# Kernel optimization log

Measured on AMD Instinct MI355X. Metric: run time of the kernel, lower is better.

## Reference

```python
import jax, jax.numpy as jnp
import numpy as np

B, T, D = 32, 2048, 80
K1 = K2 = 3
S1 = S2 = 2
CB_DIM, CB_SIZE = 512, 1024
MASK_P = 0.1
NOISE_STD = 0.1
INPUT_DIM = D * K1 * K2  # 720


def _win_idx(T_in, k, s):
    Tp = (T_in - k) // s + 1
    return jnp.arange(Tp)[:, None] * s + jnp.arange(k)[None, :]  # (Tp, k)


def _unfold(x, k, s):
    # matches torch x.unfold(1, k, s).view(B, Tp, -1): out[b, t, f*k + j] = x[b, t*s + j, f]
    idx = _win_idx(x.shape[1], k, s)
    w = x[:, idx, :]                 # (B, Tp, k, F)
    w = jnp.swapaxes(w, 2, 3)        # (B, Tp, F, k)
    return w.reshape(w.shape[0], w.shape[1], -1)


def setup_inputs() -> dict:
    key = jax.random.key(0)
    k1, k2, k3, k4, k5 = jax.random.split(key, 5)
    raw_feats = jax.random.normal(k1, (B, T, D), jnp.float32)
    auged_feats = jax.random.normal(k2, (B, T, D), jnp.float32)
    length = jax.random.randint(k3, (B,), T // 2, T + 1)
    xav = (2.0 / (INPUT_DIM + CB_DIM)) ** 0.5  # xavier_normal std
    projector = jax.random.normal(k4, (INPUT_DIM, CB_DIM), jnp.float32) * xav
    codebook = jax.random.normal(k5, (CB_SIZE, CB_DIM), jnp.float32)
    return {"raw_feats": raw_feats, "auged_feats": auged_feats, "length": length,
            "projector": projector, "codebook": codebook}


def reference(raw_feats, auged_feats, length, projector, codebook):
    T1 = (T - K1) // S1 + 1
    T2 = (T1 - K2) // S2 + 1
    idx1 = _win_idx(T, K1, S1)                         # (T1, K1)
    idx2 = _win_idx(T1, K2, S2)                        # (T2, K2)
    frame_windows = idx1[idx2].reshape(T2, K1 * K2)    # (T2, 9) original frame idx per subsampled step
    label_lengths = ((length - K1) // S1 + 1 - K2) // S2 + 1  # (B,)

    # --- label path: two torch-style unfolds -> project -> nearest codebook entry ---
    stacked = _unfold(_unfold(raw_feats, K1, S1), K2, S2)     # (B, T2, 720)
    targets = jnp.matmul(stacked, projector)                  # (B, T2, 512)
    # squared-euclidean expansion; same argmin as ||t - c||
    dist = (jnp.sum(targets * targets, axis=-1, keepdims=True)
            - 2.0 * jnp.einsum('btd,cd->btc', targets, codebook)
            + jnp.sum(codebook * codebook, axis=-1))          # (B, T2, 1024)
    labels = jnp.argmin(dist, axis=-1) + 1                    # labels start from 1; 0 = ignore idx
    valid = jnp.arange(T2)[None, :] < label_lengths[:, None]  # (B, T2)
    labels = jnp.where(valid, labels, 0)[None]                # (num_codebooks=1, B, T2)

    # --- static (span length 1) random masking on valid subsampled steps ---
    mkey = jax.random.key(42)
    km, kn = jax.random.split(mkey)
    masked = (jax.random.uniform(km, (B, T2)) < MASK_P) & valid
    masked_dim = masked.astype(jnp.float32)                   # (B, T2)
    # scatter masked subsampled steps back onto original frame indices (union of windows)
    hits = jnp.zeros((B, T), jnp.float32).at[:, frame_windows].add(masked_dim[:, :, None])
    frame_mask = hits > 0                                     # (B, T)
    noise = NOISE_STD * jax.random.normal(kn, (B, T, D), auged_feats.dtype)
    masked_feats = jnp.where(frame_mask[:, :, None], noise, auged_feats)
    return masked_feats, labels, masked_dim
```

## Files before the change

kernel.cpp:

```cpp
#include <hip/hip_runtime.h>
#include <cstdint>

#define B_    32
#define T_    2048
#define D_    80
#define T2_   511
#define NROW  16352
#define GK    720
#define CBD   512
#define CBS   1024
#define HMASK 8176
#define HN    2621440
#define NP    16384
#define KB    23

using bfrag = __attribute__((ext_vector_type(8))) short;
using f32x4 = __attribute__((ext_vector_type(4))) float;
using s8    = __attribute__((ext_vector_type(8))) short;

__device__ inline ushort f2bf(float f){
  uint32_t u = __float_as_uint(f);
  uint32_t r = (u + 0x7FFFu + ((u >> 16) & 1u)) >> 16;
  return (ushort)r;
}
__device__ inline float bf2f(ushort h){ return __uint_as_float(((uint32_t)h) << 16); }

#define GLL16(gsrc, ldst) __builtin_amdgcn_global_load_lds( \
    (__attribute__((address_space(1))) void*)(gsrc), \
    (__attribute__((address_space(3))) void*)(ldst), 16, 0, 0)

__host__ __device__ inline uint32_t rotl_(uint32_t v, int d){ return (v<<d)|(v>>(32-d)); }

__host__ __device__ inline void tf2x32(uint32_t k0, uint32_t k1, uint32_t& x0, uint32_t& x1){
  uint32_t ks2 = k0 ^ k1 ^ 0x1BD11BDAu;
  x0 += k0; x1 += k1;
  const int r0[4] = {13,15,26,6}, r1[4] = {17,29,16,24};
#pragma unroll
  for (int i=0;i<4;i++){ x0 += x1; x1 = rotl_(x1, r0[i]); x1 ^= x0; }
  x0 += k1; x1 += ks2 + 1u;
#pragma unroll
  for (int i=0;i<4;i++){ x0 += x1; x1 = rotl_(x1, r1[i]); x1 ^= x0; }
  x0 += ks2; x1 += k0 + 2u;
#pragma unroll
  for (int i=0;i<4;i++){ x0 += x1; x1 = rotl_(x1, r0[i]); x1 ^= x0; }
  x0 += k0; x1 += k1 + 3u;
#pragma unroll
  for (int i=0;i<4;i++){ x0 += x1; x1 = rotl_(x1, r1[i]); x1 ^= x0; }
  x0 += k1; x1 += ks2 + 4u;
#pragma unroll
  for (int i=0;i<4;i++){ x0 += x1; x1 = rotl_(x1, r0[i]); x1 ^= x0; }
  x0 += ks2; x1 += k0 + 5u;
}

__device__ inline float erfinv_f(float x){
  float w = -log1pf(-x*x);
  float p;
  if (w < 5.0f){
    w -= 2.5f;
    p = 2.81022636e-08f;
    p = fmaf(p, w, 3.43273939e-07f);
    p = fmaf(p, w, -3.5233877e-06f);
    p = fmaf(p, w, -4.39150654e-06f);
    p = fmaf(p, w, 0.00021858087f);
    p = fmaf(p, w, -0.00125372503f);
    p = fmaf(p, w, -0.00417768164f);
    p = fmaf(p, w, 0.246640727f);
    p = fmaf(p, w, 1.50140941f);
  } else {
    w = sqrtf(w) - 3.0f;
    p = -0.000200214257f;
    p = fmaf(p, w, 0.000100950558f);
    p = fmaf(p, w, 0.00134934322f);
    p = fmaf(p, w, -0.00367342844f);
    p = fmaf(p, w, 0.00573950773f);
    p = fmaf(p, w, -0.0076224613f);
    p = fmaf(p, w, 0.00943887047f);
    p = fmaf(p, w, 1.00167406f);
    p = fmaf(p, w, 2.83297682f);
  }
  return p * x;
}

__device__ inline int label_len(int L){ return (((L - 3) / 2) - 2) / 2 + 1; }

__global__ void cbnorm_k(const float* __restrict__ cb, ushort* __restrict__ W0, ushort* __restrict__ W1){
  int c = blockIdx.x, lane = threadIdx.x;
  double s = 0.0;
  for (int k = lane; k < CBD; k += 64){ float v = cb[c*CBD + k]; s += (double)v * (double)v; }
#pragma unroll
  for (int off = 32; off; off >>= 1) s += __shfl_down(s, off);
  float nf = (float)s;
  nf = __shfl(nf, 0);
  size_t base = ((size_t)(KB-1)*CBS + c)*32;
  int sw = ((c >> 1) & 3) << 3;
  if (lane == 16){
    float h = -0.5f * nf;
    ushort h0 = f2bf(h); ushort h1 = f2bf(h - bf2f(h0));
    W0[base + (16 ^ sw)] = h0; W1[base + (16 ^ sw)] = h1;
  } else if (lane > 16 && lane < 32){
    W0[base + (lane ^ sw)] = 0; W1[base + (lane ^ sw)] = 0;
  }
}

__global__ void gather_k(const float* __restrict__ raw, ushort* __restrict__ S0, ushort* __restrict__ S1){
  int idx = blockIdx.x * 256 + threadIdx.x;
  int g  = idx & 3;
  int n  = (idx >> 2) & (NP - 1);
  int kb = idx >> 16;
  int b = n / T2_, t2 = n - b * T2_;
  s8 o0, o1;
#pragma unroll
  for (int j = 0; j < 8; ++j){
    int k = kb*32 + g*8 + j;
    float v = 0.f;
    if (n < NROW){
      if (k < GK){
        int d = k / 9, rem = k - 9*d;
        int k1 = rem / 3, k2 = rem - 3*k1;
        int tm = 4*t2 + 2*k2 + k1;
        v = raw[(b * T_ + tm) * D_ + d];
      } else if (k == GK) v = 1.f;
    }
    ushort h0 = f2bf(v); ushort h1 = f2bf(v - bf2f(h0));
    o0[j] = (short)h0; o1[j] = (short)h1;
  }
  int gs = g ^ ((n >> 1) & 3);
  size_t off = ((size_t)kb*NP + n)*32 + gs*8;
  *(s8*)&S0[off] = o0;
  *(s8*)&S1[off] = o1;
}

__global__ __launch_bounds__(256) void wgemm_k(const float* __restrict__ P, const float* __restrict__ cb,
                                               float* __restrict__ Wp){
  __shared__ float sP[16][68];
  __shared__ float sC[16][68];
  int r0 = blockIdx.y * 64, c0 = blockIdx.x * 64;
  int kz = blockIdx.z;
  int tid = threadIdx.x, tx = tid & 15, ty = tid >> 4;
  float acc[4][4] = {};
  for (int k0 = kz * 128; k0 < kz * 128 + 128; k0 += 16){
    __syncthreads();
    {
      int r = tid >> 2, kq = tid & 3;
      int rr = r0 + r;
      float4 v = {0.f,0.f,0.f,0.f};
      if (rr < GK) v = *(const float4*)&P[rr * CBD + k0 + kq * 4];
      sP[kq*4+0][r] = v.x; sP[kq*4+1][r] = v.y; sP[kq*4+2][r] = v.z; sP[kq*4+3][r] = v.w;
      float4 w = *(const float4*)&cb[(c0 + r) * CBD + k0 + kq * 4];
      sC[kq*4+0][r] = w.x; sC[kq*4+1][r] = w.y; sC[kq*4+2][r] = w.z; sC[kq*4+3][r] = w.w;
    }
    __syncthreads();
#pragma unroll
    for (int kk = 0; kk < 16; ++kk){
      float4 a = *(const float4*)&sP[kk][ty * 4];
      float4 b = *(const float4*)&sC[kk][tx * 4];
      float av[4] = {a.x,a.y,a.z,a.w}, bv[4] = {b.x,b.y,b.z,b.w};
#pragma unroll
      for (int i = 0; i < 4; ++i)
#pragma unroll
        for (int j = 0; j < 4; ++j) acc[i][j] = fmaf(av[i], bv[j], acc[i][j]);
    }
  }
#pragma unroll
  for (int i = 0; i < 4; ++i){
    int r = r0 + ty * 4 + i;
    if (r < GK){
      float4 o; o.x = acc[i][0]; o.y = acc[i][1]; o.z = acc[i][2]; o.w = acc[i][3];
      *(float4*)&Wp[((size_t)kz * GK + r) * CBS + c0 + tx * 4] = o;
    }
  }
}

__global__ void wreduce_k(const float* __restrict__ Wp, ushort* __restrict__ W0, ushort* __restrict__ W1){
  int idx = blockIdx.x * 256 + threadIdx.x;
  int r = idx >> 10, c = idx & (CBS - 1);
  float v = Wp[(size_t)r * CBS + c]
          + Wp[((size_t)GK + r) * CBS + c]
          + Wp[((size_t)2*GK + r) * CBS + c]
          + Wp[((size_t)3*GK + r) * CBS + c];
  ushort h0 = f2bf(v); ushort h1 = f2bf(v - bf2f(h0));
  size_t o = ((size_t)(r >> 5) * CBS + c) * 32 + ((r & 31) ^ (((c >> 1) & 3) << 3));
  W0[o] = h0; W1[o] = h1;
}

__global__ __launch_bounds__(512, 2) void score_k(const ushort* __restrict__ S0, const ushort* __restrict__ S1,
                                                  const ushort* __restrict__ W0g, const ushort* __restrict__ W1g,
                                                  float* __restrict__ pval, int* __restrict__ pidx){
  __shared__ __align__(16) ushort lds[2 * 16384];
  int tid = threadIdx.x;
  int lane = tid & 63, wid = tid >> 6;
  int wm = wid >> 2, wn = wid & 3;
  int g = lane >> 4, lr = lane & 15;
  int gsw = g ^ ((lr >> 1) & 3);

  int id = blockIdx.x;
  int xcd = id & 7, slot = id >> 3;
  int cidx = slot & 3, ridx = (xcd << 3) | (slot >> 2);
  int n0 = ridx * 256, c0 = cidx * 256;

  const ushort* sbase = (wid < 4) ? (S0 + (size_t)n0*32) : (S1 + (size_t)n0*32);
  int ckbase  = (wid & 3) * 4;
  int dstbase = ((wid < 4) ? 0 : 8192) + ckbase * 512;

  size_t wofs0 = ((size_t)c0 + wn*64 + lr) * 32 + gsw * 8;

  f32x4 acc[8][4] = {};

#pragma unroll
  for (int q = 0; q < 4; ++q)
    GLL16(sbase + (size_t)(ckbase + q)*512 + lane*8, lds + dstbase + q*512);
  asm volatile("s_waitcnt vmcnt(0)" ::: "memory");
  __builtin_amdgcn_s_barrier();

  for (int kb = 0; kb < KB; ++kb){
    const ushort* cur = lds + ((kb & 1) ? 16384 : 0);
    ushort*       nxt = lds + ((kb & 1) ? 0 : 16384);

    bfrag b0c[4], b1c[4];
    {
      size_t wo = (size_t)kb * CBS * 32 + wofs0;
#pragma unroll
      for (int nt = 0; nt < 4; ++nt){
        b0c[nt] = *(const bfrag*)&W0g[wo + (size_t)nt*512];
        b1c[nt] = *(const bfrag*)&W1g[wo + (size_t)nt*512];
      }
    }
    if (kb + 1 < KB){
      const ushort* s = sbase + (size_t)(kb+1)*NP*32;
#pragma unroll
      for (int q = 0; q < 4; ++q)
        GLL16(s + (size_t)(ckbase + q)*512 + lane*8, nxt + dstbase + q*512);
    }
    bfrag a0[8], a1[8];
    {
      int abase = (wm*128 + lr)*32 + gsw*8;
#pragma unroll
      for (int mt = 0; mt < 8; ++mt){
        a0[mt] = *(const bfrag*)&cur[abase + mt*512];
        a1[mt] = *(const bfrag*)&cur[8192 + abase + mt*512];
      }
    }
#pragma unroll
    for (int hf = 0; hf < 2; ++hf){
      __builtin_amdgcn_s_setprio(1);
#pragma unroll
      for (int mtl = 0; mtl < 4; ++mtl)
#pragma unroll
        for (int nt = 0; nt < 4; ++nt)
          acc[hf*4+mtl][nt] = __builtin_amdgcn_mfma_f32_16x16x32_bf16(a0[hf*4+mtl], b0c[nt], acc[hf*4+mtl][nt], 0,0,0);
#pragma unroll
      for (int mtl = 0; mtl < 4; ++mtl)
#pragma unroll
        for (int nt = 0; nt < 4; ++nt)
          acc[hf*4+mtl][nt] = __builtin_amdgcn_mfma_f32_16x16x32_bf16(a0[hf*4+mtl], b1c[nt], acc[hf*4+mtl][nt], 0,0,0);
#pragma unroll
      for (int mtl = 0; mtl < 4; ++mtl)
#pragma unroll
        for (int nt = 0; nt < 4; ++nt)
          acc[hf*4+mtl][nt] = __builtin_amdgcn_mfma_f32_16x16x32_bf16(a1[hf*4+mtl], b0c[nt], acc[hf*4+mtl][nt], 0,0,0);
      __builtin_amdgcn_s_setprio(0);
    }
    asm volatile("s_waitcnt vmcnt(0)" ::: "memory");
    __builtin_amdgcn_s_barrier();
  }

#pragma unroll
  for (int mt = 0; mt < 8; ++mt){
    float bv[4]; int bi[4];
#pragma unroll
    for (int r = 0; r < 4; ++r){
      float best = 3.4e38f; int besti = 0;
#pragma unroll
      for (int nt = 0; nt < 4; ++nt){
        float d = -2.f * acc[mt][nt][r];
        int c = c0 + wn*64 + nt*16 + lr;
        if (d < best){ best = d; besti = c; }
      }
      bv[r] = best; bi[r] = besti;
    }
#pragma unroll
    for (int off = 1; off < 16; off <<= 1){
#pragma unroll
      for (int r = 0; r < 4; ++r){
        float ov = __shfl_xor(bv[r], off);
        int   oi = __shfl_xor(bi[r], off);
        if (ov < bv[r] || (ov == bv[r] && oi < bi[r])){ bv[r] = ov; bi[r] = oi; }
      }
    }
    if (lr == 0){
      int pp = cidx*4 + wn;
#pragma unroll
      for (int r = 0; r < 4; ++r){
        int n = n0 + wm*128 + mt*16 + g*4 + r;
        pval[(size_t)pp*NP + n] = bv[r];
        pidx[(size_t)pp*NP + n] = bi[r];
      }
    }
  }
}

__device__ inline void emit_mask(const int* len, float* md, int i, uint32_t bits){
  float u = __uint_as_float((bits >> 9) | 0x3F800000u) - 1.0f;
  int b = i / T2_, t2 = i - b * T2_;
  bool m = (u < 0.1f) && (t2 < label_len(len[b]));
  md[i] = m ? 1.0f : 0.0f;
}

__device__ inline void comb_one(const float* __restrict__ pval, const int* __restrict__ pidx,
                                const int* __restrict__ len, float* __restrict__ lb, int n){
  float bv = pval[n]; int bi = pidx[n];
#pragma unroll
  for (int p = 1; p < 16; ++p){
    float v = pval[(size_t)p*NP + n]; int ii = pidx[(size_t)p*NP + n];
    if (v < bv || (v == bv && ii < bi)){ bv = v; bi = ii; }
  }
  int b = n / T2_, t2 = n - b * T2_;
  lb[n] = (t2 < label_len(len[b])) ? (float)(bi + 1) : 0.f;
}

__global__ void maskcomb_k(const float* __restrict__ pval, const int* __restrict__ pidx,
                           const int* __restrict__ len, float* __restrict__ lb,
                           float* __restrict__ md, uint32_t km0, uint32_t km1){
  int j = blockIdx.x * 256 + threadIdx.x;
  if (j >= HMASK) return;
  uint32_t x0 = (uint32_t)j, x1 = (uint32_t)(j + HMASK);
  tf2x32(km0, km1, x0, x1);
  emit_mask(len, md, j, x0);
  emit_mask(len, md, j + HMASK, x1);
  comb_one(pval, pidx, len, lb, j);
  comb_one(pval, pidx, len, lb, j + HMASK);
}

__device__ inline bool frame_masked(const float* md, int i){
  int tabs = i / D_;
  int t = tabs & (T_ - 1);
  int b = i / (D_ * T_);
  int lo = (t < 3) ? 0 : ((t - 3) >> 2);
  int hi = t >> 2; if (hi > T2_ - 1) hi = T2_ - 1;
  bool m = false;
  for (int t2 = lo; t2 <= hi; ++t2) m = m || (md[b * T2_ + t2] != 0.f);
  return m;
}

__device__ inline float noise_from_bits(uint32_t bits){
  float f = __uint_as_float((bits >> 9) | 0x3F800000u) - 1.0f;
  const float LOV = -0.99999994f;
  float u = fmaf(f, 2.0f, LOV);
  u = fmaxf(LOV, u);
  return 0.1f * (1.41421356f * erfinv_f(u));
}

__global__ void feats_k(const float* __restrict__ aug, const float* __restrict__ md,
                        float* __restrict__ mf, uint32_t kn0, uint32_t kn1){
  int j = blockIdx.x * 256 + threadIdx.x;
  bool m1 = frame_masked(md, j);
  bool m2 = frame_masked(md, j + HN);
  if (m1 || m2){
    uint32_t x0 = (uint32_t)j, x1 = (uint32_t)(j + HN);
    tf2x32(kn0, kn1, x0, x1);
    mf[j]      = m1 ? noise_from_bits(x0) : aug[j];
    mf[j + HN] = m2 ? noise_from_bits(x1) : aug[j + HN];
  } else {
    mf[j]      = aug[j];
    mf[j + HN] = aug[j + HN];
  }
}

extern "C" void kernel_launch(void* const* d_in, const int* in_sizes, int n_in,
                              void* d_out, int out_size, void* d_ws, size_t ws_size,
                              hipStream_t stream){
  const float* raw  = (const float*)d_in[0];
  const float* aug  = (const float*)d_in[1];
  const int*   len  = (const int*)  d_in[2];
  const float* proj = (const float*)d_in[3];
  const float* cb   = (const float*)d_in[4];

  float* out = (float*)d_out;
  float* mf  = out;
  float* lb  = out + 5242880;
  float* md  = out + 5259232;

  ushort* w  = (ushort*)d_ws;
  ushort* W0 = w;
  ushort* W1 = W0 + (size_t)KB*CBS*32;
  ushort* S0 = W1 + (size_t)KB*CBS*32;
  ushort* S1 = S0 + (size_t)KB*NP*32;
  float* pval = (float*)(S1 + (size_t)KB*NP*32);
  int*   pidx = (int*)(pval + (size_t)16*NP);
  float* Wp   = (float*)(pidx + (size_t)16*NP);

  uint32_t a0 = 0u, a1 = 2u, b0 = 1u, b1 = 3u;
  tf2x32(0u, 42u, a0, a1);
  tf2x32(0u, 42u, b0, b1);
  uint32_t km0 = a0, km1 = b0, kn0 = a1, kn1 = b1;

  cbnorm_k<<<CBS, 64, 0, stream>>>(cb, W0, W1);
  wgemm_k<<<dim3(CBS / 64, 12, 4), 256, 0, stream>>>(proj, cb, Wp);
  wreduce_k<<<(GK * CBS) / 256, 256, 0, stream>>>(Wp, W0, W1);
  gather_k<<<(KB * NP * 4) / 256, 256, 0, stream>>>(raw, S0, S1);
  score_k<<<256, 512, 0, stream>>>(S0, S1, W0, W1, pval, pidx);
  maskcomb_k<<<(HMASK + 255) / 256, 256, 0, stream>>>(pval, pidx, len, lb, md, km0, km1);
  feats_k<<<HN / 256, 256, 0, stream>>>(aug, md, mf, kn0, kn1);
}
```

Before: 161.5 us.

## Stage codebook tiles in LDS for score GEMM and tile gather through shared memory

The score kernel now loads both the split-bf16 activation tiles and the split-bf16 weight tiles into a double-buffered 128KB dynamic LDS region. Previously each wave read the weight fragments straight from global memory. The MFMA loop is split into phases separated by sched and workgroup barriers, which lowers register pressure and reuses the A fragments. The gather kernel now stages a block of raw frames in LDS and has each thread write all k-blocks for its row, replacing the per-element strided global reads. This adds more barriers and LDS footprint, and occupancy may drop with 128KB of shared memory per block.

```diff
diff --git a/kernel.cpp b/kernel.cpp
--- a/kernel.cpp
+++ b/kernel.cpp
@@ -13,6 +13,7 @@
 #define HN    2621440
 #define NP    16384
 #define KB    23
+#define GLDS  (259*81*4)
 
 using bfrag = __attribute__((ext_vector_type(8))) short;
 using f32x4 = __attribute__((ext_vector_type(4))) float;
@@ -102,32 +103,46 @@
   }
 }
 
-__global__ void gather_k(const float* __restrict__ raw, ushort* __restrict__ S0, ushort* __restrict__ S1){
-  int idx = blockIdx.x * 256 + threadIdx.x;
-  int g  = idx & 3;
-  int n  = (idx >> 2) & (NP - 1);
-  int kb = idx >> 16;
-  int b = n / T2_, t2 = n - b * T2_;
-  s8 o0, o1;
-#pragma unroll
-  for (int j = 0; j < 8; ++j){
-    int k = kb*32 + g*8 + j;
-    float v = 0.f;
-    if (n < NROW){
+__global__ __launch_bounds__(256) void gather_k(const float* __restrict__ raw,
+                                                ushort* __restrict__ S0, ushort* __restrict__ S1){
+  extern __shared__ float lraw[];
+  int b = blockIdx.x >> 3, ch = blockIdx.x & 7;
+  int t20 = ch * 64;
+  int nt2 = (T2_ - t20 < 64) ? (T2_ - t20) : 64;
+  int r0 = 4 * t20;
+  int rows = (T_ - r0 < 259) ? (T_ - r0) : 259;
+  int tid = threadIdx.x;
+  const float4* gsrc = (const float4*)(raw + ((size_t)b*T_ + r0)*D_);
+  int nf4 = rows * 20;
+  for (int q = tid; q < nf4; q += 256){
+    float4 v = gsrc[q];
+    int row = q / 20, c4 = (q - row*20) * 4;
+    float* dst = &lraw[row*81 + c4];
+    dst[0]=v.x; dst[1]=v.y; dst[2]=v.z; dst[3]=v.w;
+  }
+  __syncthreads();
+  int nl = tid >> 2, g = tid & 3;
+  if (nl >= nt2) return;
+  int n = b*T2_ + t20 + nl;
+  int gs = g ^ ((n >> 1) & 3);
+  for (int kb = 0; kb < KB; ++kb){
+    s8 o0, o1;
+#pragma unroll
+    for (int j = 0; j < 8; ++j){
+      int k = kb*32 + g*8 + j;
+      float v = 0.f;
       if (k < GK){
         int d = k / 9, rem = k - 9*d;
         int k1 = rem / 3, k2 = rem - 3*k1;
-        int tm = 4*t2 + 2*k2 + k1;
-        v = raw[(b * T_ + tm) * D_ + d];
+        v = lraw[(4*nl + 2*k2 + k1)*81 + d];
       } else if (k == GK) v = 1.f;
-    }
-    ushort h0 = f2bf(v); ushort h1 = f2bf(v - bf2f(h0));
-    o0[j] = (short)h0; o1[j] = (short)h1;
-  }
-  int gs = g ^ ((n >> 1) & 3);
-  size_t off = ((size_t)kb*NP + n)*32 + gs*8;
-  *(s8*)&S0[off] = o0;
-  *(s8*)&S1[off] = o1;
+      ushort h0 = f2bf(v); ushort h1 = f2bf(v - bf2f(h0));
+      o0[j] = (short)h0; o1[j] = (short)h1;
+    }
+    size_t off = ((size_t)kb*NP + n)*32 + gs*8;
+    *(s8*)&S0[off] = o0;
+    *(s8*)&S1[off] = o1;
+  }
 }
 
 __global__ __launch_bounds__(256) void wgemm_k(const float* __restrict__ P, const float* __restrict__ cb,
@@ -184,9 +199,9 @@
 }
 
 __global__ __launch_bounds__(512, 2) void score_k(const ushort* __restrict__ S0, const ushort* __restrict__ S1,
-                                                  const ushort* __restrict__ W0g, const ushort* __restrict__ W1g,
+                                                  const ushort* __restrict__ W0, const ushort* __restrict__ W1,
                                                   float* __restrict__ pval, int* __restrict__ pidx){
-  __shared__ __align__(16) ushort lds[2 * 16384];
+  extern __shared__ ushort lds[];
   int tid = threadIdx.x;
   int lane = tid & 63, wid = tid >> 6;
   int wm = wid >> 2, wn = wid & 3;
@@ -198,70 +213,100 @@
   int cidx = slot & 3, ridx = (xcd << 3) | (slot >> 2);
   int n0 = ridx * 256, c0 = cidx * 256;
 
-  const ushort* sbase = (wid < 4) ? (S0 + (size_t)n0*32) : (S1 + (size_t)n0*32);
-  int ckbase  = (wid & 3) * 4;
-  int dstbase = ((wid < 4) ? 0 : 8192) + ckbase * 512;
-
-  size_t wofs0 = ((size_t)c0 + wn*64 + lr) * 32 + gsw * 8;
+  int p = wid >> 1, h = wid & 1;
+  const ushort* src0;
+  size_t kstride;
+  if      (p == 0){ src0 = S0 + (size_t)n0*32; kstride = (size_t)NP*32; }
+  else if (p == 1){ src0 = S1 + (size_t)n0*32; kstride = (size_t)NP*32; }
+  else if (p == 2){ src0 = W0 + (size_t)c0*32; kstride = (size_t)CBS*32; }
+  else            { src0 = W1 + (size_t)c0*32; kstride = (size_t)CBS*32; }
+  src0 += h * 4096;
+  int doff = p * 8192 + h * 4096;
 
   f32x4 acc[8][4] = {};
 
 #pragma unroll
-  for (int q = 0; q < 4; ++q)
-    GLL16(sbase + (size_t)(ckbase + q)*512 + lane*8, lds + dstbase + q*512);
-  asm volatile("s_waitcnt vmcnt(0)" ::: "memory");
-  __builtin_amdgcn_s_barrier();
+  for (int q = 0; q < 8; ++q) GLL16(src0 + q*512 + lane*8, lds + doff + q*512);
+
+  int abase = (wm*128 + lr)*32 + gsw*8;
+  int bbase = (wn*64  + lr)*32 + gsw*8;
 
   for (int kb = 0; kb < KB; ++kb){
-    const ushort* cur = lds + ((kb & 1) ? 16384 : 0);
-    ushort*       nxt = lds + ((kb & 1) ? 0 : 16384);
-
-    bfrag b0c[4], b1c[4];
-    {
-      size_t wo = (size_t)kb * CBS * 32 + wofs0;
-#pragma unroll
-      for (int nt = 0; nt < 4; ++nt){
-        b0c[nt] = *(const bfrag*)&W0g[wo + (size_t)nt*512];
-        b1c[nt] = *(const bfrag*)&W1g[wo + (size_t)nt*512];
-      }
-    }
-    if (kb + 1 < KB){
-      const ushort* s = sbase + (size_t)(kb+1)*NP*32;
-#pragma unroll
-      for (int q = 0; q < 4; ++q)
-        GLL16(s + (size_t)(ckbase + q)*512 + lane*8, nxt + dstbase + q*512);
-    }
-    bfrag a0[8], a1[8];
-    {
-      int abase = (wm*128 + lr)*32 + gsw*8;
-#pragma unroll
-      for (int mt = 0; mt < 8; ++mt){
-        a0[mt] = *(const bfrag*)&cur[abase + mt*512];
-        a1[mt] = *(const bfrag*)&cur[8192 + abase + mt*512];
-      }
-    }
-#pragma unroll
-    for (int hf = 0; hf < 2; ++hf){
-      __builtin_amdgcn_s_setprio(1);
-#pragma unroll
-      for (int mtl = 0; mtl < 4; ++mtl)
-#pragma unroll
-        for (int nt = 0; nt < 4; ++nt)
-          acc[hf*4+mtl][nt] = __builtin_amdgcn_mfma_f32_16x16x32_bf16(a0[hf*4+mtl], b0c[nt], acc[hf*4+mtl][nt], 0,0,0);
-#pragma unroll
-      for (int mtl = 0; mtl < 4; ++mtl)
-#pragma unroll
-        for (int nt = 0; nt < 4; ++nt)
-          acc[hf*4+mtl][nt] = __builtin_amdgcn_mfma_f32_16x16x32_bf16(a0[hf*4+mtl], b1c[nt], acc[hf*4+mtl][nt], 0,0,0);
-#pragma unroll
-      for (int mtl = 0; mtl < 4; ++mtl)
-#pragma unroll
-        for (int nt = 0; nt < 4; ++nt)
-          acc[hf*4+mtl][nt] = __builtin_amdgcn_mfma_f32_16x16x32_bf16(a1[hf*4+mtl], b0c[nt], acc[hf*4+mtl][nt], 0,0,0);
-      __builtin_amdgcn_s_setprio(0);
-    }
+    const ushort* cur = lds + (kb & 1) * 32768;
+    ushort*       nxt = lds + ((kb & 1) ^ 1) * 32768;
     asm volatile("s_waitcnt vmcnt(0)" ::: "memory");
     __builtin_amdgcn_s_barrier();
+
+    const ushort* A0 = cur;
+    const ushort* A1 = cur + 8192;
+    const ushort* B0 = cur + 16384;
+    const ushort* B1 = cur + 24576;
+
+    bfrag a[4], b0f[4], b1f[4];
+#pragma unroll
+    for (int mt = 0; mt < 4; ++mt) a[mt] = *(const bfrag*)&A0[abase + mt*512];
+#pragma unroll
+    for (int nt = 0; nt < 4; ++nt) b0f[nt] = *(const bfrag*)&B0[bbase + nt*512];
+    if (kb + 1 < KB){
+      const ushort* s = src0 + (size_t)(kb+1)*kstride;
+#pragma unroll
+      for (int q = 0; q < 8; ++q) GLL16(s + q*512 + lane*8, nxt + doff + q*512);
+    }
+    asm volatile("s_waitcnt lgkmcnt(0)" ::: "memory");
+    __builtin_amdgcn_sched_barrier(0);
+    __builtin_amdgcn_s_setprio(1);
+#pragma unroll
+    for (int mt = 0; mt < 4; ++mt)
+#pragma unroll
+      for (int nt = 0; nt < 4; ++nt)
+        acc[mt][nt] = __builtin_amdgcn_mfma_f32_16x16x32_bf16(a[mt], b0f[nt], acc[mt][nt], 0,0,0);
+    __builtin_amdgcn_s_setprio(0);
+    __builtin_amdgcn_sched_barrier(0);
+    __builtin_amdgcn_s_barrier();
+#pragma unroll
+    for (int nt = 0; nt < 4; ++nt) b1f[nt] = *(const bfrag*)&B1[bbase + nt*512];
+    asm volatile("s_waitcnt lgkmcnt(0)" ::: "memory");
+    __builtin_amdgcn_sched_barrier(0);
+    __builtin_amdgcn_s_setprio(1);
+#pragma unroll
+    for (int mt = 0; mt < 4; ++mt)
+#pragma unroll
+      for (int nt = 0; nt < 4; ++nt)
+        acc[mt][nt] = __builtin_amdgcn_mfma_f32_16x16x32_bf16(a[mt], b1f[nt], acc[mt][nt], 0,0,0);
+    __builtin_amdgcn_s_setprio(0);
+    __builtin_amdgcn_sched_barrier(0);
+    __builtin_amdgcn_s_barrier();
+#pragma unroll
+    for (int mt = 0; mt < 4; ++mt) a[mt] = *(const bfrag*)&A0[abase + (mt+4)*512];
+    asm volatile("s_waitcnt lgkmcnt(0)" ::: "memory");
+    __builtin_amdgcn_sched_barrier(0);
+    __builtin_amdgcn_s_setprio(1);
+#pragma unroll
+    for (int mt = 0; mt < 4; ++mt)
+#pragma unroll
+      for (int nt = 0; nt < 4; ++nt)
+        acc[4+mt][nt] = __builtin_amdgcn_mfma_f32_16x16x32_bf16(a[mt], b0f[nt], acc[4+mt][nt], 0,0,0);
+#pragma unroll
+    for (int mt = 0; mt < 4; ++mt)
+#pragma unroll
+      for (int nt = 0; nt < 4; ++nt)
+        acc[4+mt][nt] = __builtin_amdgcn_mfma_f32_16x16x32_bf16(a[mt], b1f[nt], acc[4+mt][nt], 0,0,0);
+    __builtin_amdgcn_s_setprio(0);
+    __builtin_amdgcn_sched_barrier(0);
+    __builtin_amdgcn_s_barrier();
+    bfrag a1f[8];
+#pragma unroll
+    for (int mt = 0; mt < 8; ++mt) a1f[mt] = *(const bfrag*)&A1[abase + mt*512];
+    asm volatile("s_waitcnt lgkmcnt(0)" ::: "memory");
+    __builtin_amdgcn_sched_barrier(0);
+    __builtin_amdgcn_s_setprio(1);
+#pragma unroll
+    for (int mt = 0; mt < 8; ++mt)
+#pragma unroll
+      for (int nt = 0; nt < 4; ++nt)
+        acc[mt][nt] = __builtin_amdgcn_mfma_f32_16x16x32_bf16(a1f[mt], b0f[nt], acc[mt][nt], 0,0,0);
+    __builtin_amdgcn_s_setprio(0);
+    __builtin_amdgcn_sched_barrier(0);
   }
 
 #pragma unroll
@@ -389,6 +434,9 @@
   int*   pidx = (int*)(pval + (size_t)16*NP);
   float* Wp   = (float*)(pidx + (size_t)16*NP);
 
+  hipFuncSetAttribute((const void*)score_k,  hipFuncAttributeMaxDynamicSharedMemorySize, 131072);
+  hipFuncSetAttribute((const void*)gather_k, hipFuncAttributeMaxDynamicSharedMemorySize, GLDS);
+
   uint32_t a0 = 0u, a1 = 2u, b0 = 1u, b1 = 3u;
   tf2x32(0u, 42u, a0, a1);
   tf2x32(0u, 42u, b0, b1);
@@ -397,8 +445,8 @@
   cbnorm_k<<<CBS, 64, 0, stream>>>(cb, W0, W1);
   wgemm_k<<<dim3(CBS / 64, 12, 4), 256, 0, stream>>>(proj, cb, Wp);
   wreduce_k<<<(GK * CBS) / 256, 256, 0, stream>>>(Wp, W0, W1);
-  gather_k<<<(KB * NP * 4) / 256, 256, 0, stream>>>(raw, S0, S1);
-  score_k<<<256, 512, 0, stream>>>(S0, S1, W0, W1, pval, pidx);
+  gather_k<<<256, 256, GLDS, stream>>>(raw, S0, S1);
+  score_k<<<256, 512, 131072, stream>>>(S0, S1, W0, W1, pval, pidx);
   maskcomb_k<<<(HMASK + 255) / 256, 256, 0, stream>>>(pval, pidx, len, lb, md, km0, km1);
   feats_k<<<HN / 256, 256, 0, stream>>>(aug, md, mf, kn0, kn1);
 }
```

Result: faster. 147.8 us (-8.5%).
